# Performance work log

Measured on AMD Instinct MI355X. Metric: run time of the kernel, lower is better.

## Reference

```python
import jax, jax.numpy as jnp
import numpy as np

N = 8_000_000
NUM_MOLS = 200_000

def setup_inputs() -> dict:
    key = jax.random.key(0)
    k1, k2 = jax.random.split(key)
    atoms_x = jax.random.normal(k1, (N, 3), dtype=jnp.float32)
    graph_batch = jnp.sort(jax.random.randint(k2, (N,), 0, NUM_MOLS, dtype=jnp.int64))
    return {"atoms_x": atoms_x, "graph_batch": graph_batch, "num_mols": NUM_MOLS}

def reference(atoms_x, graph_batch, num_mols):
    # Per-molecule mean via single-pass segment reduction (replaces O(N*num_mols) mask loop)
    seg_sum = jax.ops.segment_sum(atoms_x, graph_batch, num_segments=num_mols)          # [M, 3]
    counts = jax.ops.segment_sum(jnp.ones((atoms_x.shape[0],), atoms_x.dtype),
                                 graph_batch, num_segments=num_mols)                    # [M]
    mean = seg_sum / jnp.maximum(counts, 1.0)[:, None]                                  # empty mols -> 0 center
    return atoms_x - mean[graph_batch]
```

## Files before the change

kernel.cpp:

```cpp
#include <hip/hip_runtime.h>


static constexpr int WAVE   = 64;
static constexpr int WPB    = 4;
static constexpr int TPB    = WAVE * WPB;
static constexpr int CPT    = 8;
static constexpr int WCHUNK = WAVE * CPT;
static constexpr int SLOTS  = 64;

#define LDS_FENCE() asm volatile("s_waitcnt lgkmcnt(0)" ::: "memory")

__device__ void serial_fallback(const float* __restrict__ x,
                                const int* __restrict__ gb,
                                float* __restrict__ out, int n,
                                long long cs, long long ce, int lane) {
  if (lane != 0) return;
  long long i = cs;
  while (i < ce) {
    int id = gb[i];
    long long rs = i; while (rs > 0 && gb[rs - 1] == id) --rs;
    long long re = i; while (re < n && gb[re] == id) ++re;
    float sx = 0.f, sy = 0.f, sz = 0.f;
    for (long long k = rs; k < re; ++k) {
      sx += x[k * 3 + 0]; sy += x[k * 3 + 1]; sz += x[k * 3 + 2];
    }
    float inv = 1.f / (float)(re - rs);
    float mx = sx * inv, my = sy * inv, mz = sz * inv;
    long long we = (re < ce) ? re : ce;
    for (long long k = i; k < we; ++k) {
      out[k * 3 + 0] = x[k * 3 + 0] - mx;
      out[k * 3 + 1] = x[k * 3 + 1] - my;
      out[k * 3 + 2] = x[k * 3 + 2] - mz;
    }
    i = we;
  }
}

__global__ __launch_bounds__(TPB) void fused_center_kernel(
    const float* __restrict__ x, const int* __restrict__ gb,
    float* __restrict__ out, int n) {
  __shared__ float sums_all[WPB][SLOTS * 4];

  const int w = threadIdx.x >> 6;
  const int lane = threadIdx.x & 63;
  float* sums = sums_all[w];

  const long long cs = ((long long)blockIdx.x * WPB + w) * WCHUNK;
  if (cs >= (long long)n) return;
  const long long ce = (cs + WCHUNK < (long long)n) ? cs + WCHUNK : (long long)n;

  if (ce - cs < WCHUNK) {
    const int fid = gb[cs];
    const int lid = gb[ce - 1];
    const int span = lid - fid + 1;
    if (span > SLOTS) { serial_fallback(x, gb, out, n, cs, ce, lane); return; }
    for (int s = lane; s < span * 4; s += WAVE) sums[s] = 0.f;
    LDS_FENCE();
    for (long long i = cs + lane; i < ce; i += WAVE) {
      int s = (gb[i] - fid) * 4;
      atomicAdd(&sums[s + 0], x[i * 3 + 0]);
      atomicAdd(&sums[s + 1], x[i * 3 + 1]);
      atomicAdd(&sums[s + 2], x[i * 3 + 2]);
      atomicAdd(&sums[s + 3], 1.f);
    }
    if (cs > 0) {
      float hx = 0.f, hy = 0.f, hz = 0.f, hc = 0.f;
      long long off = 1 + lane;
      for (;;) {
        long long i = cs - off;
        bool m = (i >= 0) && (gb[i] == fid);
        if (m) { hx += x[i*3+0]; hy += x[i*3+1]; hz += x[i*3+2]; hc += 1.f; }
        if (__popcll(__ballot(m)) < WAVE) break;
        off += WAVE;
      }
#pragma unroll
      for (int d = 1; d < 64; d <<= 1) {
        hx += __shfl_xor(hx, d); hy += __shfl_xor(hy, d);
        hz += __shfl_xor(hz, d); hc += __shfl_xor(hc, d);
      }
      if (lane == 0 && hc > 0.f) {
        atomicAdd(&sums[0], hx); atomicAdd(&sums[1], hy);
        atomicAdd(&sums[2], hz); atomicAdd(&sums[3], hc);
      }
    }
    LDS_FENCE();
    for (int s = lane; s < span; s += WAVE) {
      float c = sums[s * 4 + 3];
      if (c > 0.f) {
        float inv = 1.f / c;
        sums[s*4+0] *= inv; sums[s*4+1] *= inv; sums[s*4+2] *= inv;
      }
    }
    LDS_FENCE();
    for (long long i = cs + lane; i < ce; i += WAVE) {
      int s = (gb[i] - fid) * 4;
      out[i * 3 + 0] = x[i * 3 + 0] - sums[s + 0];
      out[i * 3 + 1] = x[i * 3 + 1] - sums[s + 1];
      out[i * 3 + 2] = x[i * 3 + 2] - sums[s + 2];
    }
    return;
  }

  const long long base = cs + (long long)lane * CPT;

  float f[CPT * 3];
  int ids[CPT];
  {
    const float4* xv = reinterpret_cast<const float4*>(x + base * 3);
#pragma unroll
    for (int j = 0; j < CPT * 3 / 4; ++j) {
      float4 v = xv[j];
      f[j * 4 + 0] = v.x; f[j * 4 + 1] = v.y;
      f[j * 4 + 2] = v.z; f[j * 4 + 3] = v.w;
    }
    const int4* gv = reinterpret_cast<const int4*>(gb + base);
#pragma unroll
    for (int j = 0; j < CPT / 4; ++j) {
      int4 g = gv[j];
      ids[j * 4 + 0] = g.x; ids[j * 4 + 1] = g.y;
      ids[j * 4 + 2] = g.z; ids[j * 4 + 3] = g.w;
    }
  }

  const bool hasF = (cs > 0);
  const bool hasB = (ce < (long long)n);
  int pf = -1, pb = -1;
  if (hasF) pf = gb[cs - 1 - lane];
  if (hasB && ce + lane < (long long)n) pb = gb[ce + lane];

  reinterpret_cast<float4*>(sums)[lane] = make_float4(0.f, 0.f, 0.f, 0.f);
  LDS_FENCE();

  const int fid = __shfl(ids[0], 0);
  const int lid = __shfl(ids[CPT - 1], WAVE - 1);
  const int span = lid - fid + 1;
  if (span > SLOTS) { serial_fallback(x, gb, out, n, cs, ce, lane); return; }

  const bool mf = hasF && (pf == fid);
  const bool mb = hasB && (pb == lid);
  float fhx = 0.f, fhy = 0.f, fhz = 0.f, fhc = 0.f;
  if (mf) {
    long long i = cs - 1 - lane;
    fhx = x[i * 3 + 0]; fhy = x[i * 3 + 1]; fhz = x[i * 3 + 2]; fhc = 1.f;
  }
  float bhx = 0.f, bhy = 0.f, bhz = 0.f, bhc = 0.f;
  if (mb) {
    long long i = ce + lane;
    bhx = x[i * 3 + 0]; bhy = x[i * 3 + 1]; bhz = x[i * 3 + 2]; bhc = 1.f;
  }

  {
    int cur = ids[0];
    float sx = 0.f, sy = 0.f, sz = 0.f, sc = 0.f;
#pragma unroll
    for (int j = 0; j < CPT; ++j) {
      if (ids[j] != cur) {
        int s = (cur - fid) * 4;
        atomicAdd(&sums[s + 0], sx); atomicAdd(&sums[s + 1], sy);
        atomicAdd(&sums[s + 2], sz); atomicAdd(&sums[s + 3], sc);
        cur = ids[j]; sx = sy = sz = sc = 0.f;
      }
      sx += f[j * 3 + 0]; sy += f[j * 3 + 1]; sz += f[j * 3 + 2]; sc += 1.f;
    }
    int s = (cur - fid) * 4;
    atomicAdd(&sums[s + 0], sx); atomicAdd(&sums[s + 1], sy);
    atomicAdd(&sums[s + 2], sz); atomicAdd(&sums[s + 3], sc);
  }

  if (hasF) {
    unsigned long long bal = __ballot(mf);
    long long off = (long long)WAVE + 1 + lane;
    while (__popcll(bal) == WAVE) {
      long long i = cs - off;
      bool m2 = (i >= 0) && (gb[i] == fid);
      if (m2) {
        fhx += x[i*3+0]; fhy += x[i*3+1]; fhz += x[i*3+2]; fhc += 1.f;
      }
      bal = __ballot(m2);
      off += WAVE;
    }
#pragma unroll
    for (int d = 1; d < 64; d <<= 1) {
      fhx += __shfl_xor(fhx, d); fhy += __shfl_xor(fhy, d);
      fhz += __shfl_xor(fhz, d); fhc += __shfl_xor(fhc, d);
    }
    if (lane == 0 && fhc > 0.f) {
      atomicAdd(&sums[0], fhx); atomicAdd(&sums[1], fhy);
      atomicAdd(&sums[2], fhz); atomicAdd(&sums[3], fhc);
    }
  }
  if (hasB) {
    unsigned long long bal = __ballot(mb);
    long long off = (long long)WAVE + lane;
    while (__popcll(bal) == WAVE) {
      long long i = ce + off;
      bool m2 = (i < (long long)n) && (gb[i] == lid);
      if (m2) {
        bhx += x[i*3+0]; bhy += x[i*3+1]; bhz += x[i*3+2]; bhc += 1.f;
      }
      bal = __ballot(m2);
      off += WAVE;
    }
#pragma unroll
    for (int d = 1; d < 64; d <<= 1) {
      bhx += __shfl_xor(bhx, d); bhy += __shfl_xor(bhy, d);
      bhz += __shfl_xor(bhz, d); bhc += __shfl_xor(bhc, d);
    }
    if (lane == 0 && bhc > 0.f) {
      int s = (lid - fid) * 4;
      atomicAdd(&sums[s + 0], bhx); atomicAdd(&sums[s + 1], bhy);
      atomicAdd(&sums[s + 2], bhz); atomicAdd(&sums[s + 3], bhc);
    }
  }
  LDS_FENCE();

  if (lane < span) {
    float c = sums[lane * 4 + 3];
    if (c > 0.f) {
      float inv = 1.f / c;
      sums[lane*4+0] *= inv; sums[lane*4+1] *= inv; sums[lane*4+2] *= inv;
    }
  }
  LDS_FENCE();

#pragma unroll
  for (int j = 0; j < CPT; ++j) {
    int s = (ids[j] - fid) * 4;
    f[j * 3 + 0] -= sums[s + 0];
    f[j * 3 + 1] -= sums[s + 1];
    f[j * 3 + 2] -= sums[s + 2];
  }
  float4* ov = reinterpret_cast<float4*>(out + base * 3);
#pragma unroll
  for (int j = 0; j < CPT * 3 / 4; ++j)
    ov[j] = make_float4(f[j * 4 + 0], f[j * 4 + 1],
                        f[j * 4 + 2], f[j * 4 + 3]);
}

extern "C" void kernel_launch(void* const* d_in, const int* in_sizes, int n_in,
                              void* d_out, int out_size, void* d_ws, size_t ws_size,
                              hipStream_t stream) {
  const float* x = (const float*)d_in[0];
  const int* gb = (const int*)d_in[1];
  float* out = (float*)d_out;
  const int n = in_sizes[0] / 3;

  long long nchunks = ((long long)n + WCHUNK - 1) / WCHUNK;
  int blocks = (int)((nchunks + WPB - 1) / WPB);
  fused_center_kernel<<<blocks, TPB, 0, stream>>>(x, gb, out, n);
}
```

Measured before the change: 55.88 us.

## Split fused centering into a per-molecule means kernel and a subtract kernel

```diff
diff --git a/kernel.cpp b/kernel.cpp
--- a/kernel.cpp
+++ b/kernel.cpp
@@ -10,35 +10,32 @@
 
 #define LDS_FENCE() asm volatile("s_waitcnt lgkmcnt(0)" ::: "memory")
 
-__device__ void serial_fallback(const float* __restrict__ x,
-                                const int* __restrict__ gb,
-                                float* __restrict__ out, int n,
-                                long long cs, long long ce, int lane) {
+__device__ void k1_serial_fallback(const float* __restrict__ x,
+                                   const int* __restrict__ gb,
+                                   float* __restrict__ ws, int n,
+                                   long long cs, long long ce, int lane) {
   if (lane != 0) return;
   long long i = cs;
   while (i < ce) {
     int id = gb[i];
     long long rs = i; while (rs > 0 && gb[rs - 1] == id) --rs;
     long long re = i; while (re < n && gb[re] == id) ++re;
-    float sx = 0.f, sy = 0.f, sz = 0.f;
-    for (long long k = rs; k < re; ++k) {
-      sx += x[k * 3 + 0]; sy += x[k * 3 + 1]; sz += x[k * 3 + 2];
-    }
-    float inv = 1.f / (float)(re - rs);
-    float mx = sx * inv, my = sy * inv, mz = sz * inv;
-    long long we = (re < ce) ? re : ce;
-    for (long long k = i; k < we; ++k) {
-      out[k * 3 + 0] = x[k * 3 + 0] - mx;
-      out[k * 3 + 1] = x[k * 3 + 1] - my;
-      out[k * 3 + 2] = x[k * 3 + 2] - mz;
-    }
-    i = we;
-  }
-}
-
-__global__ __launch_bounds__(TPB) void fused_center_kernel(
+    if (rs >= cs) {
+      float sx = 0.f, sy = 0.f, sz = 0.f;
+      for (long long k = rs; k < re; ++k) {
+        sx += x[k * 3 + 0]; sy += x[k * 3 + 1]; sz += x[k * 3 + 2];
+      }
+      float inv = 1.f / (float)(re - rs);
+      *reinterpret_cast<float4*>(&ws[(size_t)id * 4]) =
+          make_float4(sx * inv, sy * inv, sz * inv, (float)(re - rs));
+    }
+    i = re;
+  }
+}
+
+__global__ __launch_bounds__(TPB) void k1_means(
     const float* __restrict__ x, const int* __restrict__ gb,
-    float* __restrict__ out, int n) {
+    float* __restrict__ ws, int n) {
   __shared__ float sums_all[WPB][SLOTS * 4];
 
   const int w = threadIdx.x >> 6;
@@ -53,7 +50,7 @@
     const int fid = gb[cs];
     const int lid = gb[ce - 1];
     const int span = lid - fid + 1;
-    if (span > SLOTS) { serial_fallback(x, gb, out, n, cs, ce, lane); return; }
+    if (span > SLOTS) { k1_serial_fallback(x, gb, ws, n, cs, ce, lane); return; }
     for (int s = lane; s < span * 4; s += WAVE) sums[s] = 0.f;
     LDS_FENCE();
     for (long long i = cs + lane; i < ce; i += WAVE) {
@@ -84,19 +81,14 @@
       }
     }
     LDS_FENCE();
-    for (int s = lane; s < span; s += WAVE) {
+    int s0 = 0;
+    if (cs > 0 && gb[cs - 1] == fid) s0 = 1;
+    for (int s = s0 + lane; s < span; s += WAVE) {
       float c = sums[s * 4 + 3];
-      if (c > 0.f) {
-        float inv = 1.f / c;
-        sums[s*4+0] *= inv; sums[s*4+1] *= inv; sums[s*4+2] *= inv;
-      }
-    }
-    LDS_FENCE();
-    for (long long i = cs + lane; i < ce; i += WAVE) {
-      int s = (gb[i] - fid) * 4;
-      out[i * 3 + 0] = x[i * 3 + 0] - sums[s + 0];
-      out[i * 3 + 1] = x[i * 3 + 1] - sums[s + 1];
-      out[i * 3 + 2] = x[i * 3 + 2] - sums[s + 2];
+      float inv = (c > 0.f) ? 1.f / c : 0.f;
+      *reinterpret_cast<float4*>(&ws[(size_t)(fid + s) * 4]) =
+          make_float4(sums[s*4+0] * inv, sums[s*4+1] * inv,
+                      sums[s*4+2] * inv, c);
     }
     return;
   }
@@ -134,7 +126,7 @@
   const int fid = __shfl(ids[0], 0);
   const int lid = __shfl(ids[CPT - 1], WAVE - 1);
   const int span = lid - fid + 1;
-  if (span > SLOTS) { serial_fallback(x, gb, out, n, cs, ce, lane); return; }
+  if (span > SLOTS) { k1_serial_fallback(x, gb, ws, n, cs, ce, lane); return; }
 
   const bool mf = hasF && (pf == fid);
   const bool mb = hasB && (pb == lid);
@@ -214,27 +206,48 @@
   }
   LDS_FENCE();
 
-  if (lane < span) {
-    float c = sums[lane * 4 + 3];
-    if (c > 0.f) {
-      float inv = 1.f / c;
-      sums[lane*4+0] *= inv; sums[lane*4+1] *= inv; sums[lane*4+2] *= inv;
-    }
-  }
-  LDS_FENCE();
-
-#pragma unroll
-  for (int j = 0; j < CPT; ++j) {
-    int s = (ids[j] - fid) * 4;
-    f[j * 3 + 0] -= sums[s + 0];
-    f[j * 3 + 1] -= sums[s + 1];
-    f[j * 3 + 2] -= sums[s + 2];
-  }
-  float4* ov = reinterpret_cast<float4*>(out + base * 3);
-#pragma unroll
-  for (int j = 0; j < CPT * 3 / 4; ++j)
-    ov[j] = make_float4(f[j * 4 + 0], f[j * 4 + 1],
-                        f[j * 4 + 2], f[j * 4 + 3]);
+  int s0 = (hasF && __shfl((int)mf, 0)) ? 1 : 0;
+  for (int s = s0 + lane; s < span; s += WAVE) {
+    float c = sums[s * 4 + 3];
+    float inv = (c > 0.f) ? 1.f / c : 0.f;
+    *reinterpret_cast<float4*>(&ws[(size_t)(fid + s) * 4]) =
+        make_float4(sums[s*4+0] * inv, sums[s*4+1] * inv,
+                    sums[s*4+2] * inv, c);
+  }
+}
+
+__global__ __launch_bounds__(256) void k2_subtract(
+    const float* __restrict__ x, const int* __restrict__ gb,
+    const float* __restrict__ ws, float* __restrict__ out, int n) {
+  long long t = (long long)blockIdx.x * blockDim.x + threadIdx.x;
+  long long base = t * 4;
+  if (base >= n) return;
+
+  if (base + 4 <= n) {
+    int4 g = *reinterpret_cast<const int4*>(gb + base);
+    const float4* xv = reinterpret_cast<const float4*>(x + base * 3);
+    float4 v0 = xv[0], v1 = xv[1], v2 = xv[2];
+    float4 m0 = *reinterpret_cast<const float4*>(ws + (size_t)g.x * 4);
+    float4 m1 = *reinterpret_cast<const float4*>(ws + (size_t)g.y * 4);
+    float4 m2 = *reinterpret_cast<const float4*>(ws + (size_t)g.z * 4);
+    float4 m3 = *reinterpret_cast<const float4*>(ws + (size_t)g.w * 4);
+    float4 o0, o1, o2;
+    o0.x = v0.x - m0.x; o0.y = v0.y - m0.y; o0.z = v0.z - m0.z;
+    o0.w = v0.w - m1.x;
+    o1.x = v1.x - m1.y; o1.y = v1.y - m1.z;
+    o1.z = v1.z - m2.x; o1.w = v1.w - m2.y;
+    o2.x = v2.x - m2.z;
+    o2.y = v2.y - m3.x; o2.z = v2.z - m3.y; o2.w = v2.w - m3.z;
+    float4* ov = reinterpret_cast<float4*>(out + base * 3);
+    ov[0] = o0; ov[1] = o1; ov[2] = o2;
+  } else {
+    for (long long i = base; i < n; ++i) {
+      int id = gb[i];
+      out[i * 3 + 0] = x[i * 3 + 0] - ws[(size_t)id * 4 + 0];
+      out[i * 3 + 1] = x[i * 3 + 1] - ws[(size_t)id * 4 + 1];
+      out[i * 3 + 2] = x[i * 3 + 2] - ws[(size_t)id * 4 + 2];
+    }
+  }
 }
 
 extern "C" void kernel_launch(void* const* d_in, const int* in_sizes, int n_in,
@@ -243,9 +256,14 @@
   const float* x = (const float*)d_in[0];
   const int* gb = (const int*)d_in[1];
   float* out = (float*)d_out;
+  float* ws = (float*)d_ws;
   const int n = in_sizes[0] / 3;
 
   long long nchunks = ((long long)n + WCHUNK - 1) / WCHUNK;
-  int blocks = (int)((nchunks + WPB - 1) / WPB);
-  fused_center_kernel<<<blocks, TPB, 0, stream>>>(x, gb, out, n);
-}
+  int blocks1 = (int)((nchunks + WPB - 1) / WPB);
+  k1_means<<<blocks1, TPB, 0, stream>>>(x, gb, ws, n);
+
+  long long threads2 = ((long long)n + 3) / 4;
+  int blocks2 = (int)((threads2 + 255) / 256);
+  k2_subtract<<<blocks2, 256, 0, stream>>>(x, gb, ws, out, n);
+}
```

Result: slower. 85.95 us (+53.8%).
